# Kernel optimization log

Hardware: AMD Instinct MI355X
Metric: run time of the kernel (lower is better)

The kernel has to match this reference:

```python
import jax, jax.numpy as jnp
import numpy as np

H, D = 16, 64  # heads, dim_head


def _rope(x):
    # x: (b, h, n, d). rotary-embedding-torch style: interleaved pairs, theta=10000.
    n, d = x.shape[-2], x.shape[-1]
    inv_freq = 1.0 / (10000.0 ** (jnp.arange(0, d, 2, dtype=jnp.float32) / d))  # (d/2,)
    ang = jnp.arange(n, dtype=jnp.float32)[:, None] * inv_freq[None, :]  # (n, d/2)
    cos = jnp.repeat(jnp.cos(ang), 2, axis=-1).astype(x.dtype)  # (n, d) interleaved
    sin = jnp.repeat(jnp.sin(ang), 2, axis=-1).astype(x.dtype)
    xp = x.reshape(*x.shape[:-1], d // 2, 2)
    rot = jnp.stack((-xp[..., 1], xp[..., 0]), axis=-1).reshape(x.shape)
    return x * cos + rot * sin


def setup_inputs() -> dict:
    key = jax.random.key(0)
    k1, k2, k3 = jax.random.split(key, 3)
    b, n, dim = 2, 2048, 1024
    inner = H * D
    x = jax.random.normal(k1, (b, n, dim), jnp.float32)
    w_qkv = jax.random.normal(k2, (dim, 3 * inner), jnp.float32) / np.sqrt(dim).astype(np.float32)
    w_out = jax.random.normal(k3, (inner, dim), jnp.float32) / np.sqrt(inner).astype(np.float32)
    b_out = jnp.zeros((dim,), jnp.float32)
    return {"x": x, "w_qkv": w_qkv, "w_out": w_out, "b_out": b_out}


def reference(x, w_qkv, w_out, b_out):
    b, n, _ = x.shape
    qkv = x @ w_qkv  # (b, n, 3*H*D)
    q, k, v = jnp.split(qkv, 3, axis=-1)

    def split_heads(t):
        return t.reshape(b, n, H, D).transpose(0, 2, 1, 3)  # (b, h, n, d)

    q, k, v = split_heads(q), split_heads(k), split_heads(v)
    q = _rope(q)
    k = _rope(k)
    scale = 1.0 / jnp.sqrt(jnp.asarray(D, dtype=x.dtype))
    scores = jnp.einsum('bhqd,bhkd->bhqk', q, k) * scale
    attn = jax.nn.softmax(scores, axis=-1)
    o = jnp.einsum('bhqk,bhkd->bhqd', attn, v)
    o = o.transpose(0, 2, 1, 3).reshape(b, n, H * D)
    return o @ w_out + b_out
```

## Files before the change

kernel.cpp:

```cpp
#include <hip/hip_runtime.h>
#include <math.h>

#define B_    2
#define N_    2048
#define DIM_  1024
#define H_    16
#define D_    64
#define INNER_ 1024
#define QKVC_ 3072

typedef __attribute__((ext_vector_type(8))) short short8;
typedef __attribute__((ext_vector_type(4))) short short4v;
typedef __attribute__((ext_vector_type(4))) float f32x4;
typedef __attribute__((ext_vector_type(4))) float float4v;
typedef _Float16 half8 __attribute__((ext_vector_type(8)));
typedef __fp16 fp16v2 __attribute__((ext_vector_type(2)));

union h8u { short8 s; half8 h; fp16v2 h2[4]; };
static __device__ __forceinline__ half8 s2h(short8 s) { h8u u; u.s = s; return u.h; }

static __device__ __forceinline__ unsigned short f2h(float f) {
    _Float16 h = (_Float16)f;
    unsigned short u;
    __builtin_memcpy(&u, &h, 2);
    return u;
}

static __device__ __forceinline__ void gload16(const void* g, void* l) {
    __builtin_amdgcn_global_load_lds((__attribute__((address_space(1))) void*)(g),
                                     (__attribute__((address_space(3))) void*)(l),
                                     16, 0, 0);
}

__global__ __launch_bounds__(256) void convert_all(const float* __restrict__ X,
                                                   const float* __restrict__ Wq,
                                                   const float* __restrict__ Wo,
                                                   unsigned short* __restrict__ Xh,
                                                   unsigned short* __restrict__ WqT,
                                                   unsigned short* __restrict__ WoT) {
    __shared__ unsigned short Sh[64][65];
    const int blk = blockIdx.x;
    const int tid = threadIdx.x;
    if (blk < 2048) {
        int t = blk * 256 + tid;
        size_t off = (size_t)t * 8;
        float4v a = *(const float4v*)(X + off);
        float4v b = *(const float4v*)(X + off + 4);
        short8 o;
#pragma unroll
        for (int j = 0; j < 4; ++j) {
            o[j]     = (short)f2h(a[j]);
            o[4 + j] = (short)f2h(b[j]);
        }
        *(short8*)(Xh + off) = o;
        return;
    }
    const float* W;
    unsigned short* T;
    int n0, k0, Nw;
    if (blk < 2816) {
        int g = blk - 2048;
        W = Wq; T = WqT; Nw = QKVC_;
        n0 = (g % 48) * 64; k0 = (g / 48) * 64;
    } else {
        int g = blk - 2816;
        W = Wo; T = WoT; Nw = DIM_;
        n0 = (g % 16) * 64; k0 = (g / 16) * 64;
    }
#pragma unroll
    for (int l = 0; l < 16; ++l) {
        int idx = tid + l * 256;
        int r = idx >> 6, c = idx & 63;
        Sh[c][r] = f2h(W[(size_t)(k0 + r) * Nw + n0 + c]);
    }
    __syncthreads();
#pragma unroll
    for (int l = 0; l < 16; ++l) {
        int idx = tid + l * 256;
        int r = idx >> 6, c = idx & 63;
        T[(size_t)(n0 + r) * 1024 + k0 + c] = Sh[r][c];
    }
}

#define GEMM_STAGE_H(gA, gB)                                                       \
    {                                                                              \
        int rr0 = w * 32 + (lane >> 2), rr1 = w * 32 + 16 + (lane >> 2);           \
        int kc = (lane & 3) * 8;                                                   \
        gload16(gA + (size_t)(m0 + rr0) * 1024 + k0 + kc, sA + (w * 32) * 32);     \
        gload16(gA + (size_t)(m0 + rr1) * 1024 + k0 + kc, sA + (w * 32 + 16) * 32);\
        gload16(gB + (size_t)(n0 + rr0) * 1024 + k0 + kc, sB + (w * 32) * 32);     \
        gload16(gB + (size_t)(n0 + rr1) * 1024 + k0 + kc, sB + (w * 32 + 16) * 32);\
    }

#define GEMM_BODY_H()                                                              \
    half8 af[4], bf[4];                                                            \
    _Pragma("unroll") for (int f = 0; f < 4; ++f) {                                \
        af[f] = s2h(*(const short8*)&sA[(wr + f * 16 + (lane & 15)) * 32 + (lane >> 4) * 8]); \
        bf[f] = s2h(*(const short8*)&sB[(wc + f * 16 + (lane & 15)) * 32 + (lane >> 4) * 8]); \
    }                                                                              \
    _Pragma("unroll") for (int i = 0; i < 4; ++i)                                  \
        _Pragma("unroll") for (int j = 0; j < 4; ++j)                              \
            acc[i][j] = __builtin_amdgcn_mfma_f32_16x16x32_f16(af[i], bf[j], acc[i][j], 0, 0, 0);

#define QSCALE 0.180336879963f
__global__ __launch_bounds__(256) void qkv_gemm_mfma(const unsigned short* __restrict__ Ah,
                                                     const unsigned short* __restrict__ Bh,
                                                     unsigned short* __restrict__ Qh,
                                                     unsigned short* __restrict__ Kh,
                                                     unsigned short* __restrict__ Vh) {
    __shared__ __align__(16) unsigned short sA[4096], sB[4096];
    const int tid = threadIdx.x;
    const int lane = tid & 63, w = tid >> 6;
    const int wr = (w >> 1) * 64, wc = (w & 1) * 64;
    const int m0 = blockIdx.y * 128, n0 = blockIdx.x * 128;
    f32x4 acc[4][4] = {};

    for (int k0 = 0; k0 < 1024; k0 += 32) {
        GEMM_STAGE_H(Ah, Bh);
        __syncthreads();
        GEMM_BODY_H();
        __syncthreads();
    }

    const int seg = n0 >> 10;
    const int parity = lane & 1;

#pragma unroll
    for (int i = 0; i < 4; ++i) {
        int mbase = m0 + wr + i * 16 + (lane >> 4) * 4;
#pragma unroll
        for (int j = 0; j < 4; ++j) {
            int col = n0 + wc + j * 16 + (lane & 15);
            int wcol = col & 1023;
            int h = wcol >> 6, dd = wcol & 63;
            unsigned short* dst = (seg == 0) ? Qh : (seg == 1 ? Kh : Vh);
            if (seg == 2) {
#pragma unroll
                for (int r = 0; r < 4; ++r) {
                    int row = mbase + r;
                    int b = row >> 11, n = row & (N_ - 1);
                    dst[((size_t)(b * H_ + h) * N_ + n) * D_ + dd] = f2h(acc[i][j][r]);
                }
            } else {
                float freq = __builtin_amdgcn_exp2f((float)(dd >> 1) * -0.4152410118f);
#pragma unroll
                for (int r = 0; r < 4; ++r) {
                    int row = mbase + r;
                    int b = row >> 11, n = row & (N_ - 1);
                    float ang = (float)n * freq;
                    float s = __sinf(ang);
                    float c = __cosf(ang);
                    float val = acc[i][j][r];
                    float partner = __shfl_xor(val, 1);
                    float rot = parity ? (val * c + partner * s)
                                       : (val * c - partner * s);
                    if (seg == 0) rot *= QSCALE;
                    dst[((size_t)(b * H_ + h) * N_ + n) * D_ + dd] = f2h(rot);
                }
            }
        }
    }
}

__global__ __launch_bounds__(256) void out_gemm_mfma(const unsigned short* __restrict__ Ah,
                                                     const unsigned short* __restrict__ Bh,
                                                     const float* __restrict__ bias,
                                                     float* __restrict__ C) {
    __shared__ __align__(16) unsigned short sA[4096], sB[4096];
    const int tid = threadIdx.x;
    const int lane = tid & 63, w = tid >> 6;
    const int wr = (w >> 1) * 64, wc = (w & 1) * 64;
    const int m0 = blockIdx.y * 128, n0 = blockIdx.x * 128;
    f32x4 acc[4][4] = {};

    for (int k0 = 0; k0 < 1024; k0 += 32) {
        GEMM_STAGE_H(Ah, Bh);
        __syncthreads();
        GEMM_BODY_H();
        __syncthreads();
    }

#pragma unroll
    for (int i = 0; i < 4; ++i) {
        int mbase = m0 + wr + i * 16 + (lane >> 4) * 4;
#pragma unroll
        for (int j = 0; j < 4; ++j) {
            int col = n0 + wc + j * 16 + (lane & 15);
            float bv = bias[col];
#pragma unroll
            for (int r = 0; r < 4; ++r)
                C[(size_t)(mbase + r) * DIM_ + col] = acc[i][j][r] + bv;
        }
    }
}

#define PADV 72
#define NT   (N_ / 64)
__global__ __launch_bounds__(512, 4) void attn_mfma(const unsigned short* __restrict__ Qh,
                                                    const unsigned short* __restrict__ Kh,
                                                    const unsigned short* __restrict__ Vh,
                                                    unsigned short* __restrict__ Oh) {
    __shared__ __align__(16) unsigned short Ks[2 * 64 * 64];
    __shared__ __align__(16) unsigned short Vt[3][64][PADV];
    const int tid = threadIdx.x;
    const int w = tid >> 6;
    const int l = tid & 63;
    const int lr = l & 15, lg = l >> 4;

    const int f = blockIdx.y * gridDim.x + blockIdx.x;
    const int x = f & 7, g = f >> 3;
    const int bh = x * 4 + (g >> 4);
    const int q0 = (g & 15) * 128;
    const size_t base = (size_t)bh * N_ * D_;

    const int srow = tid >> 3;
    const int scg  = tid & 7;
    const int gcg  = scg ^ (srow & 7);
    const unsigned short* ksrc = Kh + base + (size_t)srow * D_ + gcg * 8;
    unsigned short* kdst = Ks + w * 512;

    const int kb0 = lr * 64 + (lg ^ (lr & 7)) * 8;
    const int kb1 = lr * 64 + ((lg + 4) ^ (lr & 7)) * 8;

    const int skv = (tid & 31) * 2;
    const int sd0 = (tid >> 5) * 4;
    const int vpos = ((skv >> 5) * 32) + (((skv >> 2) & 3) * 8) +
                     (((skv >> 4) & 1) * 4) + (skv & 3);

    const unsigned short* qrow = Qh + base + (size_t)(q0 + w * 16 + lr) * D_ + lg * 8;
    const half8 qf0 = s2h(*(const short8*)qrow);
    const half8 qf1 = s2h(*(const short8*)(qrow + 32));

    f32x4 oacc[4] = {};
    float lsum = 0.f;
    h8u pa_prev[2];
    pa_prev[0].s = short8{0,0,0,0,0,0,0,0};
    pa_prev[1].s = short8{0,0,0,0,0,0,0,0};

    gload16(ksrc, kdst);
    {
        short4v r0 = *(const short4v*)(Vh + base + (size_t)(skv + 0) * D_ + sd0);
        short4v r1 = *(const short4v*)(Vh + base + (size_t)(skv + 1) * D_ + sd0);
#pragma unroll
        for (int j = 0; j < 4; ++j) {
            unsigned int pk = (unsigned int)(unsigned short)r0[j] |
                              ((unsigned int)(unsigned short)r1[j] << 16);
            *(unsigned int*)&Vt[0][sd0 + j][vpos] = pk;
        }
    }

    int rd = 2, cu = 0, wr_ = 1;

    for (int ti = 0; ti < NT; ++ti) {
        const int kcur = ti & 1, knxt = kcur ^ 1;
        __syncthreads();

        short4v n0v = {}, n1v = {};
        if (ti + 1 < NT) {
            gload16(ksrc + (size_t)(ti + 1) * 64 * D_, kdst + knxt * 4096);
            const unsigned short* nsrc = Vh + base + (size_t)((ti + 1) * 64 + skv) * D_ + sd0;
            n0v = *(const short4v*)nsrc;
            n1v = *(const short4v*)(nsrc + D_);
        }

        f32x4 sacc[4] = {};
        const unsigned short* kbuf = Ks + kcur * 4096;
        __builtin_amdgcn_s_setprio(1);
#pragma unroll
        for (int t = 0; t < 4; ++t) {
            half8 kf0 = s2h(*(const short8*)(kbuf + t * 1024 + kb0));
            half8 kf1 = s2h(*(const short8*)(kbuf + t * 1024 + kb1));
            sacc[t] = __builtin_amdgcn_mfma_f32_16x16x32_f16(kf0, qf0, sacc[t], 0, 0, 0);
            sacc[t] = __builtin_amdgcn_mfma_f32_16x16x32_f16(kf1, qf1, sacc[t], 0, 0, 0);
        }
        if (ti > 0) {
#pragma unroll
            for (int m2 = 0; m2 < 2; ++m2)
#pragma unroll
                for (int dt = 0; dt < 4; ++dt) {
                    half8 vf = s2h(*(const short8*)&Vt[rd][dt * 16 + lr][m2 * 32 + lg * 8]);
                    oacc[dt] = __builtin_amdgcn_mfma_f32_16x16x32_f16(pa_prev[m2].h, vf, oacc[dt], 0, 0, 0);
                }
        }
        __builtin_amdgcn_s_setprio(0);

#pragma unroll
        for (int t = 0; t < 4; ++t) {
            float e0 = __builtin_amdgcn_exp2f(sacc[t][0]);
            float e1 = __builtin_amdgcn_exp2f(sacc[t][1]);
            float e2 = __builtin_amdgcn_exp2f(sacc[t][2]);
            float e3 = __builtin_amdgcn_exp2f(sacc[t][3]);
            lsum += (e0 + e1) + (e2 + e3);
            pa_prev[t >> 1].h2[(t & 1) * 2]     = __builtin_amdgcn_cvt_pkrtz(e0, e1);
            pa_prev[t >> 1].h2[(t & 1) * 2 + 1] = __builtin_amdgcn_cvt_pkrtz(e2, e3);
        }

        if (ti + 1 < NT) {
#pragma unroll
            for (int j = 0; j < 4; ++j) {
                unsigned int pk = (unsigned int)(unsigned short)n0v[j] |
                                  ((unsigned int)(unsigned short)n1v[j] << 16);
                *(unsigned int*)&Vt[wr_][sd0 + j][vpos] = pk;
            }
        }
        int t_ = rd; rd = cu; cu = wr_; wr_ = t_;
    }

#pragma unroll
    for (int m2 = 0; m2 < 2; ++m2)
#pragma unroll
        for (int dt = 0; dt < 4; ++dt) {
            half8 vf = s2h(*(const short8*)&Vt[rd][dt * 16 + lr][m2 * 32 + lg * 8]);
            oacc[dt] = __builtin_amdgcn_mfma_f32_16x16x32_f16(pa_prev[m2].h, vf, oacc[dt], 0, 0, 0);
        }

    lsum += __shfl_xor(lsum, 16);
    lsum += __shfl_xor(lsum, 32);
    int b = bh >> 4, h = bh & 15;
#pragma unroll
    for (int r = 0; r < 4; ++r) {
        float ls = __shfl(lsum, lg * 4 + r);
        float inv = 1.0f / ls;
        size_t orow = ((size_t)b * N_ + q0 + w * 16 + lg * 4 + r) * INNER_ + h * 64 + lr;
#pragma unroll
        for (int dt = 0; dt < 4; ++dt)
            Oh[orow + 16 * dt] = f2h(oacc[dt][r] * inv);
    }
}

extern "C" void kernel_launch(void* const* d_in, const int* in_sizes, int n_in,
                              void* d_out, int out_size, void* d_ws, size_t ws_size,
                              hipStream_t stream) {
    const float* x     = (const float*)d_in[0];
    const float* w_qkv = (const float*)d_in[1];
    const float* w_out = (const float*)d_in[2];
    const float* b_out = (const float*)d_in[3];
    float* out = (float*)d_out;

    unsigned short* Xh  = (unsigned short*)d_ws;
    unsigned short* WqT = Xh + 4194304;
    unsigned short* WoT = WqT + 3145728;
    unsigned short* Qh  = WoT + 1048576;
    unsigned short* Kh  = Qh + 4194304;
    unsigned short* Vh  = Kh + 4194304;

    convert_all<<<dim3(3072), 256, 0, stream>>>(x, w_qkv, w_out, Xh, WqT, WoT);
    qkv_gemm_mfma<<<dim3(QKVC_ / 128, 32), 256, 0, stream>>>(Xh, WqT, Qh, Kh, Vh);
    attn_mfma<<<dim3(N_ / 128, B_ * H_), 512, 0, stream>>>(Qh, Kh, Vh, Xh);
    out_gemm_mfma<<<dim3(DIM_ / 128, 32), 256, 0, stream>>>(Xh, WoT, b_out, out);
}
```

Measured before the change: 126.3 us.

## Switch attention to 32x32x16 MFMA with 4 waves of 32 query rows

Rewrites the attention kernel to use 32x32x16 MFMA tiles instead of 16x16x32. Each of 4 waves now handles 32 query rows, where before each of 8 waves handled 16. The block drops from 512 to 256 threads. The P tile is kept in registers using permlane32 swaps instead of a padded layout, and V is stored in an XOR-swizzled unpadded LDS layout. The aim is fewer MFMA issues, less LDS traffic per FLOP and wider output stores, at the cost of higher register pressure and fewer threads per block.

```diff
diff --git a/kernel.cpp b/kernel.cpp
--- a/kernel.cpp
+++ b/kernel.cpp
@@ -12,12 +12,18 @@
 typedef __attribute__((ext_vector_type(8))) short short8;
 typedef __attribute__((ext_vector_type(4))) short short4v;
 typedef __attribute__((ext_vector_type(4))) float f32x4;
+typedef __attribute__((ext_vector_type(16))) float f32x16;
 typedef __attribute__((ext_vector_type(4))) float float4v;
 typedef _Float16 half8 __attribute__((ext_vector_type(8)));
 typedef __fp16 fp16v2 __attribute__((ext_vector_type(2)));
 
-union h8u { short8 s; half8 h; fp16v2 h2[4]; };
+union h8u { short8 s; half8 h; fp16v2 h2[4]; unsigned int w[4]; };
 static __device__ __forceinline__ half8 s2h(short8 s) { h8u u; u.s = s; return u.h; }
+
+union pk2u { fp16v2 h2; unsigned int u; };
+static __device__ __forceinline__ unsigned int pkrtz(float a, float b) {
+    pk2u p; p.h2 = __builtin_amdgcn_cvt_pkrtz(a, b); return p.u;
+}
 
 static __device__ __forceinline__ unsigned short f2h(float f) {
     _Float16 h = (_Float16)f;
@@ -194,18 +200,17 @@
     }
 }
 
-#define PADV 72
 #define NT   (N_ / 64)
-__global__ __launch_bounds__(512, 4) void attn_mfma(const unsigned short* __restrict__ Qh,
+__global__ __launch_bounds__(256, 2) void attn_mfma(const unsigned short* __restrict__ Qh,
                                                     const unsigned short* __restrict__ Kh,
                                                     const unsigned short* __restrict__ Vh,
                                                     unsigned short* __restrict__ Oh) {
     __shared__ __align__(16) unsigned short Ks[2 * 64 * 64];
-    __shared__ __align__(16) unsigned short Vt[3][64][PADV];
+    __shared__ __align__(16) unsigned short Vt[3][64][64];
     const int tid = threadIdx.x;
     const int w = tid >> 6;
     const int l = tid & 63;
-    const int lr = l & 15, lg = l >> 4;
+    const int lq = l & 31, hi = l >> 5;
 
     const int f = blockIdx.y * gridDim.x + blockIdx.x;
     const int x = f & 7, g = f >> 3;
@@ -214,38 +219,41 @@
     const size_t base = (size_t)bh * N_ * D_;
 
     const int srow = tid >> 3;
-    const int scg  = tid & 7;
-    const int gcg  = scg ^ (srow & 7);
+    const int gcg  = (tid & 7) ^ (srow & 7);
     const unsigned short* ksrc = Kh + base + (size_t)srow * D_ + gcg * 8;
     unsigned short* kdst = Ks + w * 512;
 
-    const int kb0 = lr * 64 + (lg ^ (lr & 7)) * 8;
-    const int kb1 = lr * 64 + ((lg + 4) ^ (lr & 7)) * 8;
+    int koff[4];
+#pragma unroll
+    for (int ds = 0; ds < 4; ++ds)
+        koff[ds] = lq * 64 + ((ds * 2 + hi) ^ (lq & 7)) * 8;
 
     const int skv = (tid & 31) * 2;
-    const int sd0 = (tid >> 5) * 4;
-    const int vpos = ((skv >> 5) * 32) + (((skv >> 2) & 3) * 8) +
-                     (((skv >> 4) & 1) * 4) + (skv & 3);
-
-    const unsigned short* qrow = Qh + base + (size_t)(q0 + w * 16 + lr) * D_ + lg * 8;
-    const half8 qf0 = s2h(*(const short8*)qrow);
-    const half8 qf1 = s2h(*(const short8*)(qrow + 32));
-
-    f32x4 oacc[4] = {};
+    const int sd0 = (tid >> 5) * 8;
+    const int vg = skv >> 3, vo = skv & 7;
+
+    const unsigned short* qptr = Qh + base + (size_t)(q0 + w * 32 + lq) * D_ + hi * 8;
+    half8 qf[4];
+#pragma unroll
+    for (int ds = 0; ds < 4; ++ds) qf[ds] = s2h(*(const short8*)(qptr + 16 * ds));
+
+    f32x16 oacc[2] = {};
     float lsum = 0.f;
-    h8u pa_prev[2];
-    pa_prev[0].s = short8{0,0,0,0,0,0,0,0};
-    pa_prev[1].s = short8{0,0,0,0,0,0,0,0};
+    unsigned int paw[16];
+#pragma unroll
+    for (int i = 0; i < 16; ++i) paw[i] = 0;
 
     gload16(ksrc, kdst);
+    gload16(ksrc + 32 * D_, kdst + 2048);
     {
-        short4v r0 = *(const short4v*)(Vh + base + (size_t)(skv + 0) * D_ + sd0);
-        short4v r1 = *(const short4v*)(Vh + base + (size_t)(skv + 1) * D_ + sd0);
-#pragma unroll
-        for (int j = 0; j < 4; ++j) {
+        short8 r0 = *(const short8*)(Vh + base + (size_t)skv * D_ + sd0);
+        short8 r1 = *(const short8*)(Vh + base + (size_t)(skv + 1) * D_ + sd0);
+#pragma unroll
+        for (int j = 0; j < 8; ++j) {
             unsigned int pk = (unsigned int)(unsigned short)r0[j] |
                               ((unsigned int)(unsigned short)r1[j] << 16);
-            *(unsigned int*)&Vt[0][sd0 + j][vpos] = pk;
+            int row = sd0 + j;
+            *(unsigned int*)&Vt[0][row][((vg ^ (row & 7)) << 3) + vo] = pk;
         }
     }
 
@@ -255,77 +263,102 @@
         const int kcur = ti & 1, knxt = kcur ^ 1;
         __syncthreads();
 
-        short4v n0v = {}, n1v = {};
+        short8 n0v = {}, n1v = {};
         if (ti + 1 < NT) {
             gload16(ksrc + (size_t)(ti + 1) * 64 * D_, kdst + knxt * 4096);
+            gload16(ksrc + (size_t)((ti + 1) * 64 + 32) * D_, kdst + knxt * 4096 + 2048);
             const unsigned short* nsrc = Vh + base + (size_t)((ti + 1) * 64 + skv) * D_ + sd0;
-            n0v = *(const short4v*)nsrc;
-            n1v = *(const short4v*)(nsrc + D_);
-        }
-
-        f32x4 sacc[4] = {};
+            n0v = *(const short8*)nsrc;
+            n1v = *(const short8*)(nsrc + D_);
+        }
+
+        f32x16 sacc[2] = {};
         const unsigned short* kbuf = Ks + kcur * 4096;
         __builtin_amdgcn_s_setprio(1);
 #pragma unroll
-        for (int t = 0; t < 4; ++t) {
-            half8 kf0 = s2h(*(const short8*)(kbuf + t * 1024 + kb0));
-            half8 kf1 = s2h(*(const short8*)(kbuf + t * 1024 + kb1));
-            sacc[t] = __builtin_amdgcn_mfma_f32_16x16x32_f16(kf0, qf0, sacc[t], 0, 0, 0);
-            sacc[t] = __builtin_amdgcn_mfma_f32_16x16x32_f16(kf1, qf1, sacc[t], 0, 0, 0);
-        }
+        for (int kvt = 0; kvt < 2; ++kvt)
+#pragma unroll
+            for (int ds = 0; ds < 4; ++ds) {
+                half8 kf = s2h(*(const short8*)(kbuf + kvt * 2048 + koff[ds]));
+                sacc[kvt] = __builtin_amdgcn_mfma_f32_32x32x16_f16(kf, qf[ds], sacc[kvt], 0, 0, 0);
+            }
         if (ti > 0) {
-#pragma unroll
-            for (int m2 = 0; m2 < 2; ++m2)
-#pragma unroll
-                for (int dt = 0; dt < 4; ++dt) {
-                    half8 vf = s2h(*(const short8*)&Vt[rd][dt * 16 + lr][m2 * 32 + lg * 8]);
-                    oacc[dt] = __builtin_amdgcn_mfma_f32_16x16x32_f16(pa_prev[m2].h, vf, oacc[dt], 0, 0, 0);
+            const unsigned short* vbuf = &Vt[rd][0][0];
+#pragma unroll
+            for (int s = 0; s < 4; ++s) {
+                h8u bw;
+#pragma unroll
+                for (int y = 0; y < 4; ++y) bw.w[y] = paw[s * 4 + y];
+#pragma unroll
+                for (int dt = 0; dt < 2; ++dt) {
+                    half8 vf = s2h(*(const short8*)(vbuf + dt * 2048 + koff[s]));
+                    oacc[dt] = __builtin_amdgcn_mfma_f32_32x32x16_f16(vf, bw.h, oacc[dt], 0, 0, 0);
                 }
+            }
         }
         __builtin_amdgcn_s_setprio(0);
 
 #pragma unroll
-        for (int t = 0; t < 4; ++t) {
-            float e0 = __builtin_amdgcn_exp2f(sacc[t][0]);
-            float e1 = __builtin_amdgcn_exp2f(sacc[t][1]);
-            float e2 = __builtin_amdgcn_exp2f(sacc[t][2]);
-            float e3 = __builtin_amdgcn_exp2f(sacc[t][3]);
-            lsum += (e0 + e1) + (e2 + e3);
-            pa_prev[t >> 1].h2[(t & 1) * 2]     = __builtin_amdgcn_cvt_pkrtz(e0, e1);
-            pa_prev[t >> 1].h2[(t & 1) * 2 + 1] = __builtin_amdgcn_cvt_pkrtz(e2, e3);
+        for (int kvt = 0; kvt < 2; ++kvt) {
+            float e[16];
+#pragma unroll
+            for (int r = 0; r < 16; ++r) {
+                e[r] = __builtin_amdgcn_exp2f(sacc[kvt][r]);
+                lsum += e[r];
+            }
+            unsigned int w0 = pkrtz(e[0], e[1]),  w1 = pkrtz(e[2], e[3]);
+            unsigned int w2 = pkrtz(e[4], e[5]),  w3 = pkrtz(e[6], e[7]);
+            unsigned int w4 = pkrtz(e[8], e[9]),  w5 = pkrtz(e[10], e[11]);
+            unsigned int w6 = pkrtz(e[12], e[13]), w7 = pkrtz(e[14], e[15]);
+            asm("v_permlane32_swap_b32 %0, %1" : "+v"(w0), "+v"(w2));
+            asm("v_permlane32_swap_b32 %0, %1" : "+v"(w1), "+v"(w3));
+            asm("v_permlane32_swap_b32 %0, %1" : "+v"(w4), "+v"(w6));
+            asm("v_permlane32_swap_b32 %0, %1" : "+v"(w5), "+v"(w7));
+            paw[kvt * 8 + 0] = w0; paw[kvt * 8 + 1] = w1;
+            paw[kvt * 8 + 2] = w2; paw[kvt * 8 + 3] = w3;
+            paw[kvt * 8 + 4] = w4; paw[kvt * 8 + 5] = w5;
+            paw[kvt * 8 + 6] = w6; paw[kvt * 8 + 7] = w7;
         }
 
         if (ti + 1 < NT) {
 #pragma unroll
-            for (int j = 0; j < 4; ++j) {
+            for (int j = 0; j < 8; ++j) {
                 unsigned int pk = (unsigned int)(unsigned short)n0v[j] |
                                   ((unsigned int)(unsigned short)n1v[j] << 16);
-                *(unsigned int*)&Vt[wr_][sd0 + j][vpos] = pk;
+                int row = sd0 + j;
+                *(unsigned int*)&Vt[wr_][row][((vg ^ (row & 7)) << 3) + vo] = pk;
             }
         }
         int t_ = rd; rd = cu; cu = wr_; wr_ = t_;
     }
 
-#pragma unroll
-    for (int m2 = 0; m2 < 2; ++m2)
-#pragma unroll
-        for (int dt = 0; dt < 4; ++dt) {
-            half8 vf = s2h(*(const short8*)&Vt[rd][dt * 16 + lr][m2 * 32 + lg * 8]);
-            oacc[dt] = __builtin_amdgcn_mfma_f32_16x16x32_f16(pa_prev[m2].h, vf, oacc[dt], 0, 0, 0);
-        }
-
-    lsum += __shfl_xor(lsum, 16);
+    {
+        const unsigned short* vbuf = &Vt[rd][0][0];
+#pragma unroll
+        for (int s = 0; s < 4; ++s) {
+            h8u bw;
+#pragma unroll
+            for (int y = 0; y < 4; ++y) bw.w[y] = paw[s * 4 + y];
+#pragma unroll
+            for (int dt = 0; dt < 2; ++dt) {
+                half8 vf = s2h(*(const short8*)(vbuf + dt * 2048 + koff[s]));
+                oacc[dt] = __builtin_amdgcn_mfma_f32_32x32x16_f16(vf, bw.h, oacc[dt], 0, 0, 0);
+            }
+        }
+    }
+
     lsum += __shfl_xor(lsum, 32);
-    int b = bh >> 4, h = bh & 15;
-#pragma unroll
-    for (int r = 0; r < 4; ++r) {
-        float ls = __shfl(lsum, lg * 4 + r);
-        float inv = 1.0f / ls;
-        size_t orow = ((size_t)b * N_ + q0 + w * 16 + lg * 4 + r) * INNER_ + h * 64 + lr;
-#pragma unroll
-        for (int dt = 0; dt < 4; ++dt)
-            Oh[orow + 16 * dt] = f2h(oacc[dt][r] * inv);
-    }
+    const float inv = 1.0f / lsum;
+    const int b = bh >> 4, h = bh & 15;
+    const size_t orow = ((size_t)b * N_ + q0 + w * 32 + lq) * INNER_ + h * 64;
+#pragma unroll
+    for (int dt = 0; dt < 2; ++dt)
+#pragma unroll
+        for (int k = 0; k < 8; ++k) {
+            unsigned int pk = pkrtz(oacc[dt][2 * k] * inv, oacc[dt][2 * k + 1] * inv);
+            int d = 32 * dt + ((2 * k) & 3) + 8 * (k >> 1) + 4 * hi;
+            *(unsigned int*)&Oh[orow + d] = pk;
+        }
 }
 
 extern "C" void kernel_launch(void* const* d_in, const int* in_sizes, int n_in,
@@ -346,6 +379,6 @@
 
     convert_all<<<dim3(3072), 256, 0, stream>>>(x, w_qkv, w_out, Xh, WqT, WoT);
     qkv_gemm_mfma<<<dim3(QKVC_ / 128, 32), 256, 0, stream>>>(Xh, WqT, Qh, Kh, Vh);
-    attn_mfma<<<dim3(N_ / 128, B_ * H_), 512, 0, stream>>>(Qh, Kh, Vh, Xh);
+    attn_mfma<<<dim3(N_ / 128, B_ * H_), 256, 0, stream>>>(Qh, Kh, Vh, Xh);
     out_gemm_mfma<<<dim3(DIM_ / 128, 32), 256, 0, stream>>>(Xh, WoT, b_out, out);
 }
```

Result: no change. 126.7 us (+0.3%).
